# Optimization experiments

Hardware: AMD Instinct MI355X
Metric: run time of the kernel (lower is better)

The kernel has to match this reference:

```python
import jax, jax.numpy as jnp
import numpy as np

K = 32
EPS = 1e-16


def setup_inputs() -> dict:
    key = jax.random.key(0)
    k1, k2, k3 = jax.random.split(key, 3)
    N_l, N_h, D, F = 8192, 32768, 3, 128
    x = jax.random.normal(k1, (N_l, F), dtype=jnp.float32)
    pos_l = jax.random.normal(k2, (N_l, D), dtype=jnp.float32)
    pos_h = jax.random.normal(k3, (N_h, D), dtype=jnp.float32)
    return {"x": x, "pos_l": pos_l, "pos_h": pos_h}


def reference(x, pos_l, pos_h):
    # Squared pairwise distances [N_h, N_l] via ||h||^2 - 2 h.l + ||l||^2
    h2 = jnp.sum(pos_h * pos_h, axis=1, keepdims=True)        # [N_h, 1]
    l2 = jnp.sum(pos_l * pos_l, axis=1)                        # [N_l]
    d2 = h2 - 2.0 * (pos_h @ pos_l.T) + l2[None, :]            # [N_h, N_l]
    # k nearest source points per target point
    neg_d2k, idx = jax.lax.top_k(-d2, K)                       # [N_h, K]
    d2k = -neg_d2k
    # Inverse squared-distance weights (torch_geometric: 1/clamp(d2, min=1e-16))
    w = 1.0 / jnp.maximum(d2k, EPS)                            # [N_h, K]
    xk = x[idx]                                                # [N_h, K, F]
    y = jnp.einsum('nk,nkf->nf', w, xk) / jnp.sum(w, axis=1, keepdims=True)
    return y
```

## Files before the change

### kernel.cpp

```cpp
#include <hip/hip_runtime.h>
#include <stdint.h>

#define NL     8192
#define NH     32768
#define FDIM   128
#define KSEL   32
#define CHUNK  1024
#define NCHUNK (NL / CHUNK)
#define QPW    4
#define NWAVES 8
#define BLOCK  (NWAVES * 64)
#define QPB    (NWAVES * QPW)
#define BUFCAP 128

typedef float f32x2 __attribute__((ext_vector_type(2)));

__device__ __forceinline__ int imin(int a, int b) { return a < b ? a : b; }
__device__ __forceinline__ int imax(int a, int b) { return a > b ? a : b; }

__device__ __forceinline__ f32x2 pk_fma_lo(f32x2 s0, f32x2 s1, f32x2 s2) {
    f32x2 d;
    asm("v_pk_fma_f32 %0, %1, %2, %3 op_sel:[0,0,0] op_sel_hi:[1,0,1]"
        : "=v"(d) : "v"(s0), "v"(s1), "v"(s2));
    return d;
}
__device__ __forceinline__ f32x2 pk_fma_hi(f32x2 s0, f32x2 s1, f32x2 s2) {
    f32x2 d;
    asm("v_pk_fma_f32 %0, %1, %2, %3 op_sel:[0,1,0] op_sel_hi:[1,1,1]"
        : "=v"(d) : "v"(s0), "v"(s1), "v"(s2));
    return d;
}

__global__ __launch_bounds__(BLOCK, 8)
void knn_interp_kernel(const float* __restrict__ x,
                       const float* __restrict__ pos_l,
                       const float* __restrict__ pos_h,
                       float* __restrict__ out)
{
    __shared__ f32x2    s_x[CHUNK/2], s_y[CHUNK/2], s_z[CHUNK/2], s_w[CHUNK/2];
    __shared__ uint16_t s_idx[QPB][BUFCAP];
    __shared__ uint32_t s_cnt[QPB];
    __shared__ float    s_wd2[QPB][KSEL];
    __shared__ uint16_t s_widx[QPB][KSEL];

    const int tid   = threadIdx.x;
    const int lane  = tid & 63;
    const int wid   = tid >> 6;
    const int qbase = blockIdx.x * QPB + wid * QPW;

    f32x2 hxq[QPW/2], hyq[QPW/2], hzq[QPW/2];
#pragma unroll
    for (int j = 0; j < QPW/2; ++j) {
        const float a0x = pos_h[(size_t)(qbase + 2*j    ) * 3 + 0];
        const float a0y = pos_h[(size_t)(qbase + 2*j    ) * 3 + 1];
        const float a0z = pos_h[(size_t)(qbase + 2*j    ) * 3 + 2];
        const float a1x = pos_h[(size_t)(qbase + 2*j + 1) * 3 + 0];
        const float a1y = pos_h[(size_t)(qbase + 2*j + 1) * 3 + 1];
        const float a1z = pos_h[(size_t)(qbase + 2*j + 1) * 3 + 2];
        hxq[j] = (f32x2){-2.0f * a0x, -2.0f * a1x};
        hyq[j] = (f32x2){-2.0f * a0y, -2.0f * a1y};
        hzq[j] = (f32x2){-2.0f * a0z, -2.0f * a1z};
    }

    f32x2 rminp[QPW];
#pragma unroll
    for (int q = 0; q < QPW; ++q) rminp[q] = (f32x2){INFINITY, INFINITY};

    for (int c = 0; c < NCHUNK; ++c) {
        __syncthreads();
        for (int i = tid; i < CHUNK/2; i += BLOCK) {
            const float* p = pos_l + (size_t)(c * CHUNK + 2 * i) * 3;
            const f32x2 A = *(const f32x2*)(p + 0);
            const f32x2 B = *(const f32x2*)(p + 2);
            const f32x2 C = *(const f32x2*)(p + 4);
            s_x[i] = (f32x2){A.x, B.y};
            s_y[i] = (f32x2){A.y, C.x};
            s_z[i] = (f32x2){B.x, C.y};
            s_w[i] = (f32x2){fmaf(A.x, A.x, fmaf(A.y, A.y, B.x * B.x)),
                             fmaf(B.y, B.y, fmaf(C.x, C.x, C.y * C.y))};
        }
        __syncthreads();
#pragma unroll
        for (int i = 0; i < CHUNK/128; ++i) {
            const int pi = i * 64 + lane;
            const f32x2 xp = s_x[pi], yp = s_y[pi], zp = s_z[pi], wp = s_w[pi];
#pragma unroll
            for (int j = 0; j < QPW/2; ++j) {
                f32x2 t0 = pk_fma_lo(xp, hxq[j], wp);
                t0 = pk_fma_lo(yp, hyq[j], t0);
                t0 = pk_fma_lo(zp, hzq[j], t0);
                rminp[2*j].x = fminf(rminp[2*j].x, t0.x);
                rminp[2*j].y = fminf(rminp[2*j].y, t0.y);
                f32x2 t1 = pk_fma_hi(xp, hxq[j], wp);
                t1 = pk_fma_hi(yp, hyq[j], t1);
                t1 = pk_fma_hi(zp, hzq[j], t1);
                rminp[2*j+1].x = fminf(rminp[2*j+1].x, t1.x);
                rminp[2*j+1].y = fminf(rminp[2*j+1].y, t1.y);
            }
        }
    }

    float tau_acc[QPW];
#pragma unroll
    for (int q = 0; q < QPW; ++q) {
        float v = fminf(rminp[q].x, rminp[q].y);
#pragma unroll
        for (int k = 2; k <= 64; k <<= 1) {
#pragma unroll
            for (int jj = k >> 1; jj >= 1; jj >>= 1) {
                const float o     = __shfl_xor(v, jj);
                const bool  up    = ((lane & k) == 0);
                const bool  lower = ((lane & jj) == 0);
                v = (lower == up) ? fminf(v, o) : fmaxf(v, o);
            }
        }
        tau_acc[q] = __shfl(v, 31) + 1e-4f;
    }

    if (tid < QPB) s_cnt[tid] = 0;

    for (int c = 0; c < NCHUNK; ++c) {
        __syncthreads();
        for (int i = tid; i < CHUNK/2; i += BLOCK) {
            const float* p = pos_l + (size_t)(c * CHUNK + 2 * i) * 3;
            const f32x2 A = *(const f32x2*)(p + 0);
            const f32x2 B = *(const f32x2*)(p + 2);
            const f32x2 C = *(const f32x2*)(p + 4);
            s_x[i] = (f32x2){A.x, B.y};
            s_y[i] = (f32x2){A.y, C.x};
            s_z[i] = (f32x2){B.x, C.y};
            s_w[i] = (f32x2){fmaf(A.x, A.x, fmaf(A.y, A.y, B.x * B.x)),
                             fmaf(B.y, B.y, fmaf(C.x, C.x, C.y * C.y))};
        }
        __syncthreads();
#pragma unroll 2
        for (int i = 0; i < CHUNK/128; ++i) {
            const int pi = i * 64 + lane;
            const f32x2 xp = s_x[pi], yp = s_y[pi], zp = s_z[pi], wp = s_w[pi];
            const int g0 = c * CHUNK + 2 * pi;
#pragma unroll
            for (int j = 0; j < QPW/2; ++j) {
                f32x2 t0 = pk_fma_lo(xp, hxq[j], wp);
                t0 = pk_fma_lo(yp, hyq[j], t0);
                t0 = pk_fma_lo(zp, hzq[j], t0);
                f32x2 t1 = pk_fma_hi(xp, hxq[j], wp);
                t1 = pk_fma_hi(yp, hyq[j], t1);
                t1 = pk_fma_hi(zp, hzq[j], t1);
                const int q0 = wid * QPW + 2*j;
                if (__any(fminf(t0.x, t0.y) <= tau_acc[2*j])) {
                    if (t0.x <= tau_acc[2*j]) {
                        const uint32_t p0 = atomicAdd(&s_cnt[q0], 1u);
                        if (p0 < BUFCAP) s_idx[q0][p0] = (uint16_t)g0;
                    }
                    if (t0.y <= tau_acc[2*j]) {
                        const uint32_t p0 = atomicAdd(&s_cnt[q0], 1u);
                        if (p0 < BUFCAP) s_idx[q0][p0] = (uint16_t)(g0 + 1);
                    }
                }
                if (__any(fminf(t1.x, t1.y) <= tau_acc[2*j+1])) {
                    if (t1.x <= tau_acc[2*j+1]) {
                        const uint32_t p0 = atomicAdd(&s_cnt[q0 + 1], 1u);
                        if (p0 < BUFCAP) s_idx[q0 + 1][p0] = (uint16_t)g0;
                    }
                    if (t1.y <= tau_acc[2*j+1]) {
                        const uint32_t p0 = atomicAdd(&s_cnt[q0 + 1], 1u);
                        if (p0 < BUFCAP) s_idx[q0 + 1][p0] = (uint16_t)(g0 + 1);
                    }
                }
            }
        }
    }

#pragma unroll 1
    for (int q = 0; q < QPW; ++q) {
        const int qq = wid * QPW + q;
        uint32_t M = s_cnt[qq];
        if (M > BUFCAP) M = BUFCAP;

        const double axd = (double)pos_h[(size_t)(qbase + q) * 3 + 0];
        const double ayd = (double)pos_h[(size_t)(qbase + q) * 3 + 1];
        const double azd = (double)pos_h[(size_t)(qbase + q) * 3 + 2];

        const int i0 = ((uint32_t)(2 * lane)     < M) ? (int)s_idx[qq][2 * lane]     : -1;
        const int i1 = ((uint32_t)(2 * lane + 1) < M) ? (int)s_idx[qq][2 * lane + 1] : -1;
        float f0 = INFINITY, f1 = INFINITY;
        if (i0 >= 0) {
            const double dx = (double)pos_l[i0 * 3 + 0] - axd;
            const double dy = (double)pos_l[i0 * 3 + 1] - ayd;
            const double dz = (double)pos_l[i0 * 3 + 2] - azd;
            f0 = (float)(dx * dx + dy * dy + dz * dz);
        }
        if (i1 >= 0) {
            const double dx = (double)pos_l[i1 * 3 + 0] - axd;
            const double dy = (double)pos_l[i1 * 3 + 1] - ayd;
            const double dz = (double)pos_l[i1 * 3 + 2] - azd;
            f1 = (float)(dx * dx + dy * dy + dz * dz);
        }

        int v0 = __float_as_int(f0);
        int v1 = __float_as_int(f1);
#pragma unroll
        for (int k = 2; k <= 128; k <<= 1) {
            const bool up = ((lane & (k >> 1)) == 0);
#pragma unroll
            for (int j = k >> 1; j >= 2; j >>= 1) {
                const int  xo    = j >> 1;
                const bool lower = ((lane & xo) == 0);
                const int o0 = __shfl_xor(v0, xo);
                const int o1 = __shfl_xor(v1, xo);
                v0 = (lower == up) ? imin(v0, o0) : imax(v0, o0);
                v1 = (lower == up) ? imin(v1, o1) : imax(v1, o1);
            }
            const int mn = imin(v0, v1), mx = imax(v0, v1);
            v0 = up ? mn : mx;
            v1 = up ? mx : mn;
        }
        const int tau32 = __shfl(v1, 15);

        const bool a0 = (i0 >= 0) && (__float_as_int(f0) <= tau32);
        const bool a1 = (i1 >= 0) && (__float_as_int(f1) <= tau32);
        const unsigned long long b0 = __ballot(a0);
        const unsigned long long b1 = __ballot(a1);
        const unsigned long long mb = (lane == 63) ? 0x7FFFFFFFFFFFFFFFull
                                                   : ((1ull << (lane + 1)) - 1ull) >> 1;
        const int base = __popcll(b0 & mb) + __popcll(b1 & mb);
        const int p0 = base;
        const int p1 = base + (a0 ? 1 : 0);
        if (a0 && p0 < KSEL) { s_wd2[qq][p0] = f0; s_widx[qq][p0] = (uint16_t)i0; }
        if (a1 && p1 < KSEL) { s_wd2[qq][p1] = f1; s_widx[qq][p1] = (uint16_t)i1; }
    }

#pragma unroll 1
    for (int q = 0; q < QPW; ++q) {
        const int qq = wid * QPW + q;
        const int gq = qbase + q;
        f32x2 acc = (f32x2){0.0f, 0.0f};
        float wsum = 0.0f;
#pragma unroll 8
        for (int kk = 0; kk < KSEL; ++kk) {
            const float d2 = s_wd2[qq][kk];
            const float w  = __builtin_amdgcn_rcpf(fmaxf(d2, 1e-16f));
            const int  idx = (int)s_widx[qq][kk];
            const f32x2 r2 = *(const f32x2*)(x + (size_t)idx * FDIM + 2 * lane);
            acc.x = fmaf(w, r2.x, acc.x);
            acc.y = fmaf(w, r2.y, acc.y);
            wsum += w;
        }
        const float invw = __builtin_amdgcn_rcpf(wsum);
        *(f32x2*)(out + (size_t)gq * FDIM + 2 * lane) = (f32x2){acc.x * invw, acc.y * invw};
    }
}

extern "C" void kernel_launch(void* const* d_in, const int* in_sizes, int n_in,
                              void* d_out, int out_size, void* d_ws, size_t ws_size,
                              hipStream_t stream) {
    const float* x     = (const float*)d_in[0];
    const float* pos_l = (const float*)d_in[1];
    const float* pos_h = (const float*)d_in[2];
    float* out = (float*)d_out;
    dim3 grid(NH / QPB);
    dim3 block(BLOCK);
    hipLaunchKernelGGL(knn_interp_kernel, grid, block, 0, stream,
                       x, pos_l, pos_h, out);
}
```

Measured before the change: 178.7 us.

## Replace brute-force kNN scan with Morton-grid spatial binning and pruned search

Adds a preprocessing pipeline (init, count, scan, scatter) that bins source points into a 16^3 Morton-ordered grid with per-parent bounding boxes. A new query kernel seeds a distance bound from 64 nearby points, culls parent cells by box distance, and keeps a wave-wide sorted top-64 list only over surviving candidates. This removes the full N_h x N_l distance sweep, at the cost of four extra small launches, serial scan work and data-dependent control flow. It falls back to the old kernel when workspace is missing, and its correctness relies on the fixed grid range and the 64-candidate seed bound.

```diff
diff --git a/kernel.cpp b/kernel.cpp
--- a/kernel.cpp
+++ b/kernel.cpp
@@ -1,10 +1,308 @@
 #include <hip/hip_runtime.h>
 #include <stdint.h>
 
-#define NL     8192
-#define NH     32768
-#define FDIM   128
-#define KSEL   32
+#define NL    8192
+#define NH    32768
+#define FDIM  128
+#define KSEL  32
+
+#define GLO   (-4.0f)
+#define GINV  (2.0f)
+
+typedef float f32x2 __attribute__((ext_vector_type(2)));
+typedef float f32x4 __attribute__((ext_vector_type(4)));
+typedef unsigned long long u64;
+
+__device__ __forceinline__ int imin(int a, int b) { return a < b ? a : b; }
+__device__ __forceinline__ int imax(int a, int b) { return a > b ? a : b; }
+__device__ __forceinline__ u64 umin64(u64 a, u64 b) { return a < b ? a : b; }
+__device__ __forceinline__ u64 umax64(u64 a, u64 b) { return a > b ? a : b; }
+
+#define WS_P4    0
+#define WS_PBLO  32768
+#define WS_PBHI  34816
+#define WS_OFF   36864
+#define WS_POFF  38916
+#define WS_CNT   39176
+#define WS_FLOATS 43272
+#define WS_BYTES  (WS_FLOATS * 4)
+
+__device__ __forceinline__ uint32_t ordf(float f) {
+    uint32_t u = __float_as_uint(f);
+    return (u & 0x80000000u) ? ~u : (u | 0x80000000u);
+}
+__device__ __forceinline__ float iordf(uint32_t e) {
+    return (e & 0x80000000u) ? __uint_as_float(e & 0x7FFFFFFFu)
+                             : __uint_as_float(~e);
+}
+__device__ __forceinline__ int cellcoord(float p) {
+    return imin(imax((int)floorf((p - GLO) * GINV), 0), 15);
+}
+__device__ __forceinline__ int mort12(int ix, int iy, int iz) {
+    int m = 0;
+#pragma unroll
+    for (int b = 0; b < 4; ++b)
+        m |= (((ix >> b) & 1) << (3 * b + 2)) |
+             (((iy >> b) & 1) << (3 * b + 1)) |
+             (((iz >> b) & 1) << (3 * b));
+    return m;
+}
+__device__ __forceinline__ float dist2f(f32x4 p, float qx, float qy, float qz) {
+    const float dx = qx - p.x, dy = qy - p.y, dz = qz - p.z;
+    return fmaf(dx, dx, fmaf(dy, dy, dz * dz));
+}
+
+__global__ __launch_bounds__(256)
+void k_init(float* __restrict__ ws) {
+    const int t = blockIdx.x * 256 + threadIdx.x;
+    uint32_t* cnt = (uint32_t*)(ws + WS_CNT);
+    uint32_t* elo = (uint32_t*)(ws + WS_PBLO);
+    uint32_t* ehi = (uint32_t*)(ws + WS_PBHI);
+    if (t < 4096) cnt[t] = 0u;
+    if (t < 2048) { elo[t] = 0xFFFFFFFFu; ehi[t] = 0u; }
+}
+
+__global__ __launch_bounds__(256)
+void k_count(const float* __restrict__ pos_l, float* __restrict__ ws) {
+    const int e = blockIdx.x * 256 + threadIdx.x;
+    if (e >= NL) return;
+    const float px = pos_l[e * 3 + 0];
+    const float py = pos_l[e * 3 + 1];
+    const float pz = pos_l[e * 3 + 2];
+    const int cell = mort12(cellcoord(px), cellcoord(py), cellcoord(pz));
+    uint32_t* cnt = (uint32_t*)(ws + WS_CNT);
+    uint32_t* elo = (uint32_t*)(ws + WS_PBLO);
+    uint32_t* ehi = (uint32_t*)(ws + WS_PBHI);
+    atomicAdd(&cnt[cell], 1u);
+    const int par = cell >> 3;
+    atomicMin(&elo[par * 4 + 0], ordf(px));
+    atomicMin(&elo[par * 4 + 1], ordf(py));
+    atomicMin(&elo[par * 4 + 2], ordf(pz));
+    atomicMax(&ehi[par * 4 + 0], ordf(px));
+    atomicMax(&ehi[par * 4 + 1], ordf(py));
+    atomicMax(&ehi[par * 4 + 2], ordf(pz));
+}
+
+__global__ __launch_bounds__(1024)
+void k_scan(float* __restrict__ ws) {
+    __shared__ uint32_t s_c[1024];
+    const int tid = threadIdx.x;
+    uint32_t* cnt = (uint32_t*)(ws + WS_CNT);
+    uint16_t* off16  = (uint16_t*)(ws + WS_OFF);
+    uint16_t* poff16 = (uint16_t*)(ws + WS_POFF);
+
+    const int base = tid * 4;
+    const uint32_t v0 = cnt[base + 0], v1 = cnt[base + 1];
+    const uint32_t v2 = cnt[base + 2], v3 = cnt[base + 3];
+    const uint32_t s = v0 + v1 + v2 + v3;
+    s_c[tid] = s;
+    __syncthreads();
+    for (int o = 1; o < 1024; o <<= 1) {
+        const uint32_t t = (tid >= o) ? s_c[tid - o] : 0u;
+        __syncthreads();
+        s_c[tid] += t;
+        __syncthreads();
+    }
+    uint32_t p = s_c[tid] - s;
+    if ((tid & 1) == 0) poff16[tid >> 1] = (uint16_t)p;
+    if (tid == 0)       poff16[512]      = (uint16_t)NL;
+    off16[base + 0] = (uint16_t)p;           p += v0;
+    off16[base + 1] = (uint16_t)p;           p += v1;
+    off16[base + 2] = (uint16_t)p;           p += v2;
+    off16[base + 3] = (uint16_t)p;
+    if (tid == 1023) off16[4096] = (uint16_t)NL;
+    cnt[base + 0] = 0u; cnt[base + 1] = 0u; cnt[base + 2] = 0u; cnt[base + 3] = 0u;
+
+    if (tid < 512) {
+        uint32_t* elo = (uint32_t*)(ws + WS_PBLO);
+        uint32_t* ehi = (uint32_t*)(ws + WS_PBHI);
+        float* flo = ws + WS_PBLO;
+        float* fhi = ws + WS_PBHI;
+        const bool empty = (ehi[tid * 4 + 0] == 0u);
+#pragma unroll
+        for (int d = 0; d < 3; ++d) {
+            const float lo = empty ?  1e30f : iordf(elo[tid * 4 + d]);
+            const float hi = empty ? -1e30f : iordf(ehi[tid * 4 + d]);
+            flo[tid * 4 + d] = lo;
+            fhi[tid * 4 + d] = hi;
+        }
+        flo[tid * 4 + 3] = 0.0f;
+        fhi[tid * 4 + 3] = 0.0f;
+    }
+}
+
+__global__ __launch_bounds__(256)
+void k_scatter(const float* __restrict__ pos_l, float* __restrict__ ws) {
+    const int e = blockIdx.x * 256 + threadIdx.x;
+    if (e >= NL) return;
+    const float px = pos_l[e * 3 + 0];
+    const float py = pos_l[e * 3 + 1];
+    const float pz = pos_l[e * 3 + 2];
+    const int cell = mort12(cellcoord(px), cellcoord(py), cellcoord(pz));
+    uint32_t* cnt = (uint32_t*)(ws + WS_CNT);
+    const uint16_t* off16 = (const uint16_t*)(ws + WS_OFF);
+    const uint32_t r = atomicAdd(&cnt[cell], 1u);
+    const int pos = (int)off16[cell] + (int)r;
+    f32x4* p4 = (f32x4*)(ws + WS_P4);
+    f32x4 o; o.x = px; o.y = py; o.z = pz; o.w = __int_as_float(e);
+    p4[pos] = o;
+}
+
+#define QBLK 4
+#define INFKEY 0xFFFFFFFFFFFFFFFFull
+
+__global__ __launch_bounds__(256, 6)
+void query_kernel(const float* __restrict__ x,
+                  const float* __restrict__ pos_h,
+                  const float* __restrict__ ws,
+                  float* __restrict__ out)
+{
+    __shared__ float    s_blo[512][4];
+    __shared__ float    s_bhi[512][4];
+    __shared__ uint16_t s_poff[516];
+    __shared__ uint16_t s_pl[QBLK][512];
+    __shared__ float    s_wwt[QBLK][KSEL];
+    __shared__ uint16_t s_worig[QBLK][KSEL];
+
+    const int tid  = threadIdx.x;
+    const int lane = tid & 63;
+    const int wid  = tid >> 6;
+    const int gq   = blockIdx.x * QBLK + wid;
+
+    for (int i = tid; i < 2048; i += 256) {
+        ((float*)s_blo)[i] = ws[WS_PBLO + i];
+        ((float*)s_bhi)[i] = ws[WS_PBHI + i];
+    }
+    {
+        const uint16_t* pg = (const uint16_t*)(ws + WS_POFF);
+        for (int i = tid; i < 513; i += 256) s_poff[i] = pg[i];
+    }
+    __syncthreads();
+
+    const f32x4* p4 = (const f32x4*)(ws + WS_P4);
+    const float qx = pos_h[(size_t)gq * 3 + 0];
+    const float qy = pos_h[(size_t)gq * 3 + 1];
+    const float qz = pos_h[(size_t)gq * 3 + 2];
+    const unsigned long long lt = (1ull << lane) - 1ull;
+
+    const int qcell = mort12(cellcoord(qx), cellcoord(qy), cellcoord(qz));
+    const uint16_t* off16g = (const uint16_t*)(ws + WS_OFF);
+    const int w0 = imin(imax((int)off16g[qcell] - 24, 0), NL - 64);
+    {
+        float v = dist2f(p4[w0 + lane], qx, qy, qz);
+#pragma unroll
+        for (int k2 = 2; k2 <= 64; k2 <<= 1) {
+#pragma unroll
+            for (int jj = k2 >> 1; jj >= 1; jj >>= 1) {
+                const float o     = __shfl_xor(v, jj);
+                const bool  up    = ((lane & k2) == 0);
+                const bool  lower = ((lane & jj) == 0);
+                v = (lower == up) ? fminf(v, o) : fmaxf(v, o);
+            }
+        }
+        const float tau0 = __shfl(v, 31);
+        const float tau0m = tau0 * 1.00002f + 1e-6f;
+
+        int npar = 0;
+#pragma unroll
+        for (int r = 0; r < 8; ++r) {
+            const int c = r * 64 + lane;
+            const float ddx = fmaxf(fmaxf(s_blo[c][0] - qx, qx - s_bhi[c][0]), 0.0f);
+            const float ddy = fmaxf(fmaxf(s_blo[c][1] - qy, qy - s_bhi[c][1]), 0.0f);
+            const float ddz = fmaxf(fmaxf(s_blo[c][2] - qz, qz - s_bhi[c][2]), 0.0f);
+            const float dmin = fmaf(ddx, ddx, fmaf(ddy, ddy, ddz * ddz));
+            const bool pass = (dmin <= tau0m);
+            const unsigned long long m = __ballot(pass);
+            if (pass) s_pl[wid][npar + (int)__popcll(m & lt)] = (uint16_t)c;
+            npar += (int)__popcll(m);
+        }
+
+        u64 L = INFKEY;
+        for (int pi = 0; pi < npar; ++pi) {
+            const int par = (int)s_pl[wid][pi];
+            const int a = (int)s_poff[par];
+            const int n = (int)s_poff[par + 1] - a;
+            for (int r = 0; r < n; r += 64) {
+                const int j = r + lane;
+                u64 b = INFKEY;
+                if (j < n) {
+                    const int slot = a + j;
+                    const float d2 = dist2f(p4[slot], qx, qy, qz);
+                    b = (((u64)__float_as_uint(d2)) << 16) | (u64)slot;
+                }
+                const u64 worst = __shfl(L, 63);
+                if (!__any(b < worst)) continue;
+#pragma unroll
+                for (int k2 = 2; k2 <= 64; k2 <<= 1) {
+#pragma unroll
+                    for (int jj = k2 >> 1; jj >= 1; jj >>= 1) {
+                        const u64  o     = __shfl_xor(b, jj);
+                        const bool up    = ((lane & k2) == 0);
+                        const bool lower = ((lane & jj) == 0);
+                        b = (lower == up) ? umin64(b, o) : umax64(b, o);
+                    }
+                }
+                L = umin64(L, __shfl_xor(b, 63));
+#pragma unroll
+                for (int jj = 32; jj >= 1; jj >>= 1) {
+                    const u64 o = __shfl_xor(L, jj);
+                    L = ((lane & jj) == 0) ? umin64(L, o) : umax64(L, o);
+                }
+            }
+        }
+
+        const double axd = (double)qx, ayd = (double)qy, azd = (double)qz;
+        const bool valid = (L != INFKEY);
+        const int  slot  = (int)(L & 0xFFFFull);
+        float fd2 = INFINITY;
+        if (valid) {
+            const f32x4 p = p4[slot];
+            const double dx = (double)p.x - axd;
+            const double dy = (double)p.y - ayd;
+            const double dz = (double)p.z - azd;
+            fd2 = (float)(dx * dx + dy * dy + dz * dz);
+        }
+        u64 k2v = (((u64)__float_as_uint(fd2)) << 16)
+                | (u64)(valid ? slot : 0xFFFF);
+#pragma unroll
+        for (int k2 = 2; k2 <= 64; k2 <<= 1) {
+#pragma unroll
+            for (int jj = k2 >> 1; jj >= 1; jj >>= 1) {
+                const u64  o     = __shfl_xor(k2v, jj);
+                const bool up    = ((lane & k2) == 0);
+                const bool lower = ((lane & jj) == 0);
+                k2v = (lower == up) ? umin64(k2v, o) : umax64(k2v, o);
+            }
+        }
+        float wgt = 0.0f;
+        int   worig = 0;
+        if (lane < KSEL) {
+            const int   wslot = (int)(k2v & 0xFFFFull);
+            const float d2w   = __uint_as_float((uint32_t)(k2v >> 16));
+            worig = __float_as_int(p4[wslot].w);
+            wgt   = __builtin_amdgcn_rcpf(fmaxf(d2w, 1e-16f));
+        }
+        float wsum = wgt;
+#pragma unroll
+        for (int d = 1; d < 32; d <<= 1) wsum += __shfl_xor(wsum, d);
+        if (lane < KSEL) {
+            s_wwt[wid][lane]   = wgt * __builtin_amdgcn_rcpf(wsum);
+            s_worig[wid][lane] = (uint16_t)worig;
+        }
+    }
+
+    f32x2 acc = (f32x2){0.0f, 0.0f};
+#pragma unroll 8
+    for (int kk = 0; kk < KSEL; ++kk) {
+        const float w    = s_wwt[wid][kk];
+        const int   orig = (int)s_worig[wid][kk];
+        const f32x2 r2 = *(const f32x2*)(x + (size_t)orig * FDIM + 2 * lane);
+        acc.x = fmaf(w, r2.x, acc.x);
+        acc.y = fmaf(w, r2.y, acc.y);
+    }
+    *(f32x2*)(out + (size_t)gq * FDIM + 2 * lane) = acc;
+}
+
 #define CHUNK  1024
 #define NCHUNK (NL / CHUNK)
 #define QPW    4
@@ -12,11 +310,6 @@
 #define BLOCK  (NWAVES * 64)
 #define QPB    (NWAVES * QPW)
 #define BUFCAP 128
-
-typedef float f32x2 __attribute__((ext_vector_type(2)));
-
-__device__ __forceinline__ int imin(int a, int b) { return a < b ? a : b; }
-__device__ __forceinline__ int imax(int a, int b) { return a > b ? a : b; }
 
 __device__ __forceinline__ f32x2 pk_fma_lo(f32x2 s0, f32x2 s1, f32x2 s2) {
     f32x2 d;
@@ -61,7 +354,6 @@
         hyq[j] = (f32x2){-2.0f * a0y, -2.0f * a1y};
         hzq[j] = (f32x2){-2.0f * a0z, -2.0f * a1z};
     }
-
     f32x2 rminp[QPW];
 #pragma unroll
     for (int q = 0; q < QPW; ++q) rminp[q] = (f32x2){INFINITY, INFINITY};
@@ -99,7 +391,6 @@
             }
         }
     }
-
     float tau_acc[QPW];
 #pragma unroll
     for (int q = 0; q < QPW; ++q) {
@@ -116,9 +407,7 @@
         }
         tau_acc[q] = __shfl(v, 31) + 1e-4f;
     }
-
     if (tid < QPB) s_cnt[tid] = 0;
-
     for (int c = 0; c < NCHUNK; ++c) {
         __syncthreads();
         for (int i = tid; i < CHUNK/2; i += BLOCK) {
@@ -170,17 +459,14 @@
             }
         }
     }
-
 #pragma unroll 1
     for (int q = 0; q < QPW; ++q) {
         const int qq = wid * QPW + q;
         uint32_t M = s_cnt[qq];
         if (M > BUFCAP) M = BUFCAP;
-
         const double axd = (double)pos_h[(size_t)(qbase + q) * 3 + 0];
         const double ayd = (double)pos_h[(size_t)(qbase + q) * 3 + 1];
         const double azd = (double)pos_h[(size_t)(qbase + q) * 3 + 2];
-
         const int i0 = ((uint32_t)(2 * lane)     < M) ? (int)s_idx[qq][2 * lane]     : -1;
         const int i1 = ((uint32_t)(2 * lane + 1) < M) ? (int)s_idx[qq][2 * lane + 1] : -1;
         float f0 = INFINITY, f1 = INFINITY;
@@ -196,7 +482,6 @@
             const double dz = (double)pos_l[i1 * 3 + 2] - azd;
             f1 = (float)(dx * dx + dy * dy + dz * dz);
         }
-
         int v0 = __float_as_int(f0);
         int v1 = __float_as_int(f1);
 #pragma unroll
@@ -216,7 +501,6 @@
             v1 = up ? mx : mn;
         }
         const int tau32 = __shfl(v1, 15);
-
         const bool a0 = (i0 >= 0) && (__float_as_int(f0) <= tau32);
         const bool a1 = (i1 >= 0) && (__float_as_int(f1) <= tau32);
         const unsigned long long b0 = __ballot(a0);
@@ -229,7 +513,6 @@
         if (a0 && p0 < KSEL) { s_wd2[qq][p0] = f0; s_widx[qq][p0] = (uint16_t)i0; }
         if (a1 && p1 < KSEL) { s_wd2[qq][p1] = f1; s_widx[qq][p1] = (uint16_t)i1; }
     }
-
 #pragma unroll 1
     for (int q = 0; q < QPW; ++q) {
         const int qq = wid * QPW + q;
@@ -247,7 +530,8 @@
             wsum += w;
         }
         const float invw = __builtin_amdgcn_rcpf(wsum);
-        *(f32x2*)(out + (size_t)gq * FDIM + 2 * lane) = (f32x2){acc.x * invw, acc.y * invw};
+        out[(size_t)gq * FDIM + 2 * lane]     = acc.x * invw;
+        out[(size_t)gq * FDIM + 2 * lane + 1] = acc.y * invw;
     }
 }
 
@@ -258,8 +542,17 @@
     const float* pos_l = (const float*)d_in[1];
     const float* pos_h = (const float*)d_in[2];
     float* out = (float*)d_out;
-    dim3 grid(NH / QPB);
-    dim3 block(BLOCK);
-    hipLaunchKernelGGL(knn_interp_kernel, grid, block, 0, stream,
-                       x, pos_l, pos_h, out);
-}
+
+    if (d_ws != nullptr && ws_size >= (size_t)WS_BYTES) {
+        float* ws = (float*)d_ws;
+        hipLaunchKernelGGL(k_init,    dim3(16), dim3(256),  0, stream, ws);
+        hipLaunchKernelGGL(k_count,   dim3(32), dim3(256),  0, stream, pos_l, ws);
+        hipLaunchKernelGGL(k_scan,    dim3(1),  dim3(1024), 0, stream, ws);
+        hipLaunchKernelGGL(k_scatter, dim3(32), dim3(256),  0, stream, pos_l, ws);
+        hipLaunchKernelGGL(query_kernel, dim3(NH / QBLK), dim3(256), 0, stream,
+                           x, pos_h, ws, out);
+    } else {
+        hipLaunchKernelGGL(knn_interp_kernel, dim3(NH / QPB), dim3(BLOCK), 0, stream,
+                           x, pos_l, pos_h, out);
+    }
+}
```

Result: slower. 574.0 us (+221.1%).
